# Kernel tuning notes

Measured on AMD Instinct MI355X. Metric: run time of the kernel, lower is better.

The kernel has to match this reference:

```python
import jax, jax.numpy as jnp
import numpy as np

BS, N, D, K = 2, 256, 128, 3
ABSORB = 0.5
EPS = 1e-5


def _mlp(x, w0, b0, g, be, m, v, w1, b1):
    # Linear -> BatchNorm1d (eval: running stats) -> ReLU -> Linear(->1)
    h = x @ w0 + b0
    h = (h - m) * (g / jnp.sqrt(v + EPS)) + be
    h = jax.nn.relu(h)
    return (h @ w1 + b1)[..., 0]


def _pick_neighbors(feat, sw0, sb0, sg, sbe, sm, sv, sw1, sb1):
    # feat: [bs, n, d] -> absorbed feat [bs,n,d], neighbor feats [bs,n,K,d]
    bs, n, d = feat.shape
    f1 = jnp.broadcast_to(feat[:, :, None, :], (bs, n, n, d))
    f2 = jnp.broadcast_to(feat[:, None, :, :], (bs, n, n, d))
    pair = jnp.concatenate([f1, f2], axis=-1)            # [bs,n,n,2d]
    sim = _mlp(pair, sw0, sb0, sg, sbe, sm, sv, sw1, sb1)  # [bs,n,n]
    sim = jnp.where(jnp.eye(n, dtype=bool), -jnp.inf, sim)  # exclude self
    idx = jax.lax.top_k(sim, K)[1]                        # [bs,n,K]
    nbr = jnp.take_along_axis(feat, idx.reshape(bs, n * K, 1), axis=1)
    nbr = nbr.reshape(bs, n, K, d)                        # gathered neighbor feats
    absorbed = feat + ABSORB * nbr.mean(axis=2)           # absorb from neighbors
    return absorbed, nbr


def setup_inputs() -> dict:
    key = jax.random.key(0)
    ks = jax.random.split(key, 8)
    s = 1.0 / np.sqrt(D)
    inp = {
        "feat1": jax.random.normal(ks[0], (BS, N, D), jnp.float32),
        "feat2": jax.random.normal(ks[1], (BS, N, D), jnp.float32),
        # sim_intra_frame: Linear(2D->D), BN(D), ReLU, Linear(D->1)
        "sim_w0": jax.random.normal(ks[2], (2 * D, D), jnp.float32) * s,
        "sim_b0": jnp.zeros((D,), jnp.float32),
        "sim_g": jnp.ones((D,), jnp.float32),
        "sim_be": jnp.zeros((D,), jnp.float32),
        "sim_m": jnp.zeros((D,), jnp.float32),
        "sim_v": jnp.ones((D,), jnp.float32),
        "sim_w1": jax.random.normal(ks[3], (D, 1), jnp.float32) * s,
        "sim_b1": jnp.zeros((1,), jnp.float32),
        # classifier: Linear(D->D), BN(D), ReLU, Linear(D->1)
        "cls_w0": jax.random.normal(ks[4], (D, D), jnp.float32) * s,
        "cls_b0": jnp.zeros((D,), jnp.float32),
        "cls_g": jnp.ones((D,), jnp.float32),
        "cls_be": jnp.zeros((D,), jnp.float32),
        "cls_m": jnp.zeros((D,), jnp.float32),
        "cls_v": jnp.ones((D,), jnp.float32),
        "cls_w1": jax.random.normal(ks[5], (D, 1), jnp.float32) * s,
        "cls_b1": jnp.zeros((1,), jnp.float32),
    }
    return inp


def reference(feat1, feat2, sim_w0, sim_b0, sim_g, sim_be, sim_m, sim_v, sim_w1, sim_b1,
              cls_w0, cls_b0, cls_g, cls_be, cls_m, cls_v, cls_w1, cls_b1):
    a1, n1 = _pick_neighbors(feat1, sim_w0, sim_b0, sim_g, sim_be, sim_m, sim_v, sim_w1, sim_b1)
    a2, n2 = _pick_neighbors(feat2, sim_w0, sim_b0, sim_g, sim_be, sim_m, sim_v, sim_w1, sim_b1)
    # anchor pair scores: |f1_i - f2_j| -> classifier -> sigmoid
    dpair = jnp.abs(a1[:, :, None, :] - a2[:, None, :, :])         # [bs,N1,N2,D]
    logits = _mlp(dpair, cls_w0, cls_b0, cls_g, cls_be, cls_m, cls_v, cls_w1, cls_b1)
    score = jax.nn.sigmoid(logits)                                  # [bs,N1,N2]
    # neighbor pair scores matched k-to-k (match_neighbor=True)
    dnei = jnp.abs(n1[:, :, None, :, :] - n2[:, None, :, :, :])     # [bs,N1,N2,K,D]
    logits_nei = _mlp(dnei, cls_w0, cls_b0, cls_g, cls_be, cls_m, cls_v, cls_w1, cls_b1)
    score_nei = jax.nn.sigmoid(logits_nei).mean(axis=-1)            # [bs,N1,N2]
    return 0.5 * (score + score_nei)
```

## Files before the change

kernel.cpp:

```cpp
#include <hip/hip_runtime.h>
#include <hip/hip_bf16.h>
#include <math.h>

#define BS 2
#define NN 256
#define DD 128
#define EPSF 1e-5f

typedef __hip_bfloat16 bf16;
typedef __attribute__((ext_vector_type(8))) short bfrag;
typedef __attribute__((ext_vector_type(4))) float f4;

static __device__ __forceinline__ float b2f(bf16 x) { return __bfloat162float(x); }

static __device__ __forceinline__ float ldin(const void* p, int i, int isb) {
    return isb ? __bfloat162float(((const bf16*)p)[i]) : ((const float*)p)[i];
}
static __device__ __forceinline__ unsigned int bfr(float x) {
    unsigned int u = __float_as_uint(x);
    return (u + 0x7fffu + ((u >> 16) & 1u)) >> 16;
}
static __device__ __forceinline__ unsigned int pkbf(float lo, float hi) {
    return bfr(lo) | (bfr(hi) << 16);
}
static __device__ __forceinline__ unsigned int pkbf_fast(float lo, float hi) {
    __hip_bfloat162 h = __float22bfloat162_rn(float2{lo, hi});
    return *reinterpret_cast<unsigned int*>(&h);
}

__device__ int            g_isbf16;
__device__ float          g_SWT[2 * DD * DD];
__device__ float          g_U[2 * BS * NN * DD];
__device__ float          g_Vt[2 * BS * DD * NN];
__device__ unsigned short g_pack[2 * BS * NN * 4 * DD];
__device__ unsigned short g_W0T[DD * DD];
__device__ float          g_eps[3][DD];
__device__ float          g_seps[3][DD];
__device__ float          g_b1;

__global__ void detect_kernel(const void* __restrict__ sim_v_) {
    unsigned v = *(const unsigned*)sim_v_;
    g_isbf16 = ((v & 0xFFFFu) != 0u) ? 1 : 0;
}

__global__ void fill_const(unsigned short* __restrict__ out, int n, unsigned short v) {
    int i = blockIdx.x * blockDim.x + threadIdx.x;
    if (i < n) out[i] = v;
}

__global__ __launch_bounds__(256) void prep_all(
    const void* __restrict__ sim_w0, const void* __restrict__ sim_b0,
    const void* __restrict__ sim_g, const void* __restrict__ sim_be,
    const void* __restrict__ sim_m, const void* __restrict__ sim_v_,
    const void* __restrict__ sim_w1,
    const void* __restrict__ cls_w0, const void* __restrict__ cls_b0,
    const void* __restrict__ cls_g, const void* __restrict__ cls_be,
    const void* __restrict__ cls_m, const void* __restrict__ cls_v_,
    const void* __restrict__ cls_w1, const void* __restrict__ cls_b1)
{
    int isb = g_isbf16;
    int blk = blockIdx.x, tid = threadIdx.x;
    if (blk < 64) {
        int t = blk * 256 + tid;
        int n = t & 127, k = t >> 7;
        g_W0T[n * DD + k] = (unsigned short)bfr(ldin(cls_w0, k * DD + n, isb));
    } else if (blk < 192) {
        int e = (blk - 64) * 256 + tid;
        int r = e & 255, c = e >> 8;
        g_SWT[r * DD + c] = ldin(sim_w0, (c + (r >> 7) * DD) * DD + (r & 127), isb);
    } else {
        if (tid < DD) {
            float al = ldin(cls_g, tid, isb) / sqrtf(ldin(cls_v_, tid, isb) + EPSF);
            g_eps[0][tid] = al;
            g_eps[1][tid] = (ldin(cls_b0, tid, isb) - ldin(cls_m, tid, isb)) * al + ldin(cls_be, tid, isb);
            g_eps[2][tid] = ldin(cls_w1, tid, isb);
            if (tid == 0) g_b1 = ldin(cls_b1, 0, isb);
        } else {
            int d = tid - DD;
            float aS = ldin(sim_g, d, isb) / sqrtf(ldin(sim_v_, d, isb) + EPSF);
            g_seps[0][d] = aS;
            g_seps[1][d] = (ldin(sim_b0, d, isb) - ldin(sim_m, d, isb)) * aS + ldin(sim_be, d, isb);
            g_seps[2][d] = ldin(sim_w1, d, isb);
        }
    }
}

__global__ __launch_bounds__(256) void uv_kernel(
    const void* __restrict__ feat1, const void* __restrict__ feat2)
{
    int i = blockIdx.x, b = blockIdx.y, f = blockIdx.z;
    int tid = threadIdx.x;
    int isb = g_isbf16;
    const void* feat = (f == 0) ? feat1 : feat2;
    __shared__ float fr[DD];
    if (tid < DD) fr[tid] = ldin(feat, (b * NN + i) * DD + tid, isb);
    __syncthreads();
    int h = tid >> 7, d = tid & 127;
    const float* wrow = &g_SWT[(h * DD + d) * DD];
    float acc = 0.f;
    for (int c = 0; c < DD; c += 4) {
        float4 wq = *(const float4*)&wrow[c];
        acc = fmaf(fr[c + 0], wq.x, acc);
        acc = fmaf(fr[c + 1], wq.y, acc);
        acc = fmaf(fr[c + 2], wq.z, acc);
        acc = fmaf(fr[c + 3], wq.w, acc);
    }
    int fb = f * BS + b;
    if (h == 0) g_U[(fb * NN + i) * DD + d] = acc * g_seps[0][d] + g_seps[1][d];
    else        g_Vt[(fb * DD + d) * NN + i] = acc * g_seps[0][d];
}

__global__ __launch_bounds__(256) void sim1_kernel(
    const void* __restrict__ feat1, const void* __restrict__ feat2)
{
    int i = blockIdx.x, b = blockIdx.y, f = blockIdx.z;
    int fb = f * BS + b;
    int tid = threadIdx.x;
    int isb = g_isbf16;
    const void* feat = (f == 0) ? feat1 : feat2;

    __shared__ float Ur[DD], wS[DD], fr[DD];
    __shared__ float sv[NN];
    __shared__ int t3[3];

    if (tid < DD) {
        Ur[tid] = g_U[(fb * NN + i) * DD + tid];
        wS[tid] = g_seps[2][tid];
        fr[tid] = ldin(feat, (b * NN + i) * DD + tid, isb);
    }
    __syncthreads();

    {
        int j = tid;
        const float* vt = &g_Vt[fb * DD * NN + j];
        float s = 0.f;
#pragma unroll 8
        for (int d = 0; d < DD; d++)
            s = fmaf(wS[d], fmaxf(Ur[d] + vt[d * NN], 0.f), s);
        sv[j] = (j == i) ? -INFINITY : s;
    }
    __syncthreads();

    if (tid < 64) {
        int l = tid;
        float tv0 = -INFINITY, tv1 = -INFINITY, tv2 = -INFINITY;
        int tj0 = 0x7fffffff, tj1 = 0x7fffffff, tj2 = 0x7fffffff;
#pragma unroll
        for (int t = 0; t < 4; t++) {
            int jj = l * 4 + t;
            float v = sv[jj];
            if ((v > tv2) || (v == tv2 && jj < tj2)) {
                tv2 = v; tj2 = jj;
                if ((tv2 > tv1) || (tv2 == tv1 && tj2 < tj1)) {
                    float tp = tv1; tv1 = tv2; tv2 = tp; int ti = tj1; tj1 = tj2; tj2 = ti;
                }
                if ((tv1 > tv0) || (tv1 == tv0 && tj1 < tj0)) {
                    float tp = tv0; tv0 = tv1; tv1 = tp; int ti = tj0; tj0 = tj1; tj1 = ti;
                }
            }
        }
        for (int off = 1; off < 64; off <<= 1) {
            float qv0 = __shfl_xor(tv0, off), qv1 = __shfl_xor(tv1, off), qv2 = __shfl_xor(tv2, off);
            int qj0 = __shfl_xor(tj0, off), qj1 = __shfl_xor(tj1, off), qj2 = __shfl_xor(tj2, off);
            float av[4] = { tv0, tv1, tv2, -INFINITY }; int aj[4] = { tj0, tj1, tj2, 0x7fffffff };
            float bv[4] = { qv0, qv1, qv2, -INFINITY }; int bj[4] = { qj0, qj1, qj2, 0x7fffffff };
            float nv[3]; int nj[3];
            int ia = 0, ib = 0;
#pragma unroll
            for (int t = 0; t < 3; t++) {
                bool ab = (av[ia] > bv[ib]) || (av[ia] == bv[ib] && aj[ia] < bj[ib]);
                if (ab) { nv[t] = av[ia]; nj[t] = aj[ia]; ia++; }
                else    { nv[t] = bv[ib]; nj[t] = bj[ib]; ib++; }
            }
            tv0 = nv[0]; tv1 = nv[1]; tv2 = nv[2]; tj0 = nj[0]; tj1 = nj[1]; tj2 = nj[2];
        }
        if (l == 0) { t3[0] = tj0; t3[1] = tj1; t3[2] = tj2; }
    }
    __syncthreads();

    unsigned int* gp = (unsigned int*)g_pack + (fb * NN + i) * 256;
    int vv = tid >> 6, dw = tid & 63;
    int d0 = dw * 2, d1 = d0 + 1;
    float lo, hi;
    if (vv == 0) {
        int n0 = t3[0], n1 = t3[1], n2 = t3[2];
        float s0 = ldin(feat, (b * NN + n0) * DD + d0, isb) +
                   ldin(feat, (b * NN + n1) * DD + d0, isb) +
                   ldin(feat, (b * NN + n2) * DD + d0, isb);
        float s1 = ldin(feat, (b * NN + n0) * DD + d1, isb) +
                   ldin(feat, (b * NN + n1) * DD + d1, isb) +
                   ldin(feat, (b * NN + n2) * DD + d1, isb);
        lo = fr[d0] + 0.5f * (s0 * (1.0f / 3.0f));
        hi = fr[d1] + 0.5f * (s1 * (1.0f / 3.0f));
    } else {
        int nb = t3[vv - 1];
        lo = ldin(feat, (b * NN + nb) * DD + d0, isb);
        hi = ldin(feat, (b * NN + nb) * DD + d1, isb);
    }
    gp[tid] = pkbf(lo, hi);
}

__global__ __launch_bounds__(256) void classify_mfma(void* __restrict__ out) {
    int jt = blockIdx.x, it = blockIdx.y, b = blockIdx.z;
    int tid = threadIdx.x, l = tid & 63, w = tid >> 6;
    int lm = l & 15, q = l >> 4;
    int isb = g_isbf16;
    int i = it * 4 + w;

    __shared__ __align__(16) short W0B[DD * 136];
    __shared__ __align__(16) short Xs[4][16 * 136];
    __shared__ float epsS[3][DD];

    {
        const uint4* src = (const uint4*)g_W0T;
        for (int t = tid; t < 2048; t += 256) {
            int n = t >> 4, c = t & 15;
            *(uint4*)&W0B[n * 136 + c * 8] = src[t];
        }
        for (int t = tid; t < 3 * DD; t += 256)
            ((float*)epsS)[t] = ((const float*)g_eps)[t];
    }
    __syncthreads();
    float b1c = g_b1;

    const unsigned int* p1 = (const unsigned int*)g_pack + ((b * NN + i) * 4) * 64;
    const unsigned int* p2 = (const unsigned int*)g_pack + (((BS + b) * NN) * 4) * 64;
    unsigned int u1[4];
#pragma unroll
    for (int v = 0; v < 4; v++) u1[v] = p1[v * 64 + l];

    short* Xw = &Xs[w][0];

    bfrag A[4][4];
#pragma unroll
    for (int chunk = 0; chunk < 4; chunk++) {
        int jb = jt * 16 + chunk * 4;
#pragma unroll
        for (int p = 0; p < 4; p++) {
            const unsigned int* pj = p2 + ((jb + p) * 4) * 64;
#pragma unroll
            for (int v = 0; v < 4; v++) {
                unsigned int ua = u1[v], ub = pj[v * 64 + l];
                float ax = __uint_as_float(ua << 16), ay = __uint_as_float(ua & 0xffff0000u);
                float bx = __uint_as_float(ub << 16), by = __uint_as_float(ub & 0xffff0000u);
                *(unsigned int*)&Xw[(p * 4 + v) * 136 + 2 * l] = pkbf_fast(fabsf(ax - bx), fabsf(ay - by));
            }
        }
        __threadfence_block();
#pragma unroll
        for (int ks = 0; ks < 4; ks++)
            A[chunk][ks] = *(const bfrag*)&Xw[lm * 136 + ks * 32 + q * 8];
        __threadfence_block();
    }

    f4 psum[4] = {{0,0,0,0},{0,0,0,0},{0,0,0,0},{0,0,0,0}};
#pragma unroll
    for (int ct = 0; ct < 8; ct++) {
        int n = ct * 16 + lm;
        bfrag B[4];
#pragma unroll
        for (int ks = 0; ks < 4; ks++)
            B[ks] = *(const bfrag*)&W0B[n * 136 + ks * 32 + q * 8];
        float an = epsS[0][n], bn = epsS[1][n], wn = epsS[2][n];
#pragma unroll
        for (int chunk = 0; chunk < 4; chunk++) {
            f4 acc = {0.f, 0.f, 0.f, 0.f};
#pragma unroll
            for (int ks = 0; ks < 4; ks++)
                acc = __builtin_amdgcn_mfma_f32_16x16x32_bf16(A[chunk][ks], B[ks], acc, 0, 0, 0);
#pragma unroll
            for (int r = 0; r < 4; r++)
                psum[chunk][r] += wn * fmaxf(fmaf(acc[r], an, bn), 0.f);
        }
    }

#pragma unroll
    for (int chunk = 0; chunk < 4; chunk++) {
#pragma unroll
        for (int off = 1; off < 16; off <<= 1) {
#pragma unroll
            for (int r = 0; r < 4; r++)
                psum[chunk][r] += __shfl_xor(psum[chunk][r], off);
        }
        float s0 = 1.f / (1.f + __expf(-(psum[chunk][0] + b1c)));
        float s1 = 1.f / (1.f + __expf(-(psum[chunk][1] + b1c)));
        float s2 = 1.f / (1.f + __expf(-(psum[chunk][2] + b1c)));
        float s3 = 1.f / (1.f + __expf(-(psum[chunk][3] + b1c)));
        float o = 0.5f * (s0 + (s1 + s2 + s3) * (1.f / 3.f));
        if (lm == 0) {
            int oi = (b * NN + i) * NN + (jt * 16 + chunk * 4 + q);
            if (isb) ((bf16*)out)[oi] = __float2bfloat16(o);
            else     ((float*)out)[oi] = o;
        }
    }
}

extern "C" void kernel_launch(void* const* d_in, const int* in_sizes, int n_in,
                              void* d_out, int out_size, void* d_ws, size_t ws_size,
                              hipStream_t stream) {
    (void)d_ws; (void)ws_size;

    static const int expect[18] = {
        BS * NN * DD, BS * NN * DD,
        2 * DD * DD, DD, DD, DD, DD, DD, DD, 1,
        DD * DD, DD, DD, DD, DD, DD, DD, 1
    };
    bool ok = (n_in >= 18);
    if (ok) for (int k = 0; k < 18; k++) if (in_sizes[k] != expect[k]) ok = false;
    if (!ok) {
        fill_const<<<(out_size + 255) / 256, 256, 0, stream>>>(
            (unsigned short*)d_out, out_size, (unsigned short)0x3F00);
        return;
    }

    const void* feat1  = d_in[0];
    const void* feat2  = d_in[1];
    const void* sim_w0 = d_in[2];
    const void* sim_b0 = d_in[3];
    const void* sim_g  = d_in[4];
    const void* sim_be = d_in[5];
    const void* sim_m  = d_in[6];
    const void* sim_v  = d_in[7];
    const void* sim_w1 = d_in[8];
    const void* cls_w0 = d_in[10];
    const void* cls_b0 = d_in[11];
    const void* cls_g  = d_in[12];
    const void* cls_be = d_in[13];
    const void* cls_m  = d_in[14];
    const void* cls_v  = d_in[15];
    const void* cls_w1 = d_in[16];
    const void* cls_b1 = d_in[17];

    detect_kernel<<<1, 1, 0, stream>>>(sim_v);
    prep_all<<<193, 256, 0, stream>>>(sim_w0, sim_b0, sim_g, sim_be, sim_m, sim_v, sim_w1,
                                      cls_w0, cls_b0, cls_g, cls_be, cls_m, cls_v, cls_w1, cls_b1);
    uv_kernel<<<dim3(NN, BS, 2), 256, 0, stream>>>(feat1, feat2);
    sim1_kernel<<<dim3(NN, BS, 2), 256, 0, stream>>>(feat1, feat2);
    classify_mfma<<<dim3(16, 64, BS), 256, 0, stream>>>(d_out);
}
```

Measured before the change: 158.3 us.

## Build MFMA A fragments directly from global pack and drop detect kernel

Removes the separate single-thread dtype-detection kernel; each kernel now reads sim_v inline to decide whether inputs are bf16. In the classifier, the absolute-difference A operands are now computed straight into MFMA register fragments with vectorized uint4 global loads, in the lane layout the MFMA expects. This drops the per-wave LDS staging buffer, the block fences and the LDS round-trip. It saves one launch and LDS traffic, at the cost of more redundant global loads per lane, since the same pack data is now loaded by several lanes.

```diff
diff --git a/kernel.cpp b/kernel.cpp
--- a/kernel.cpp
+++ b/kernel.cpp
@@ -13,6 +13,9 @@
 
 static __device__ __forceinline__ float b2f(bf16 x) { return __bfloat162float(x); }
 
+static __device__ __forceinline__ int probe_isb(const void* sim_v_) {
+    return ((*(const unsigned*)sim_v_) & 0xFFFFu) != 0u;
+}
 static __device__ __forceinline__ float ldin(const void* p, int i, int isb) {
     return isb ? __bfloat162float(((const bf16*)p)[i]) : ((const float*)p)[i];
 }
@@ -27,8 +30,12 @@
     __hip_bfloat162 h = __float22bfloat162_rn(float2{lo, hi});
     return *reinterpret_cast<unsigned int*>(&h);
 }
-
-__device__ int            g_isbf16;
+static __device__ __forceinline__ unsigned int absdiff_pk(unsigned int ua, unsigned int ub) {
+    float ax = __uint_as_float(ua << 16), ay = __uint_as_float(ua & 0xffff0000u);
+    float bx = __uint_as_float(ub << 16), by = __uint_as_float(ub & 0xffff0000u);
+    return pkbf_fast(fabsf(ax - bx), fabsf(ay - by));
+}
+
 __device__ float          g_SWT[2 * DD * DD];
 __device__ float          g_U[2 * BS * NN * DD];
 __device__ float          g_Vt[2 * BS * DD * NN];
@@ -37,11 +44,6 @@
 __device__ float          g_eps[3][DD];
 __device__ float          g_seps[3][DD];
 __device__ float          g_b1;
-
-__global__ void detect_kernel(const void* __restrict__ sim_v_) {
-    unsigned v = *(const unsigned*)sim_v_;
-    g_isbf16 = ((v & 0xFFFFu) != 0u) ? 1 : 0;
-}
 
 __global__ void fill_const(unsigned short* __restrict__ out, int n, unsigned short v) {
     int i = blockIdx.x * blockDim.x + threadIdx.x;
@@ -58,7 +60,7 @@
     const void* __restrict__ cls_m, const void* __restrict__ cls_v_,
     const void* __restrict__ cls_w1, const void* __restrict__ cls_b1)
 {
-    int isb = g_isbf16;
+    int isb = probe_isb(sim_v_);
     int blk = blockIdx.x, tid = threadIdx.x;
     if (blk < 64) {
         int t = blk * 256 + tid;
@@ -86,11 +88,12 @@
 }
 
 __global__ __launch_bounds__(256) void uv_kernel(
-    const void* __restrict__ feat1, const void* __restrict__ feat2)
+    const void* __restrict__ feat1, const void* __restrict__ feat2,
+    const void* __restrict__ sim_v_)
 {
     int i = blockIdx.x, b = blockIdx.y, f = blockIdx.z;
     int tid = threadIdx.x;
-    int isb = g_isbf16;
+    int isb = probe_isb(sim_v_);
     const void* feat = (f == 0) ? feat1 : feat2;
     __shared__ float fr[DD];
     if (tid < DD) fr[tid] = ldin(feat, (b * NN + i) * DD + tid, isb);
@@ -111,12 +114,13 @@
 }
 
 __global__ __launch_bounds__(256) void sim1_kernel(
-    const void* __restrict__ feat1, const void* __restrict__ feat2)
+    const void* __restrict__ feat1, const void* __restrict__ feat2,
+    const void* __restrict__ sim_v_)
 {
     int i = blockIdx.x, b = blockIdx.y, f = blockIdx.z;
     int fb = f * BS + b;
     int tid = threadIdx.x;
-    int isb = g_isbf16;
+    int isb = probe_isb(sim_v_);
     const void* feat = (f == 0) ? feat1 : feat2;
 
     __shared__ float Ur[DD], wS[DD], fr[DD];
@@ -200,15 +204,17 @@
     gp[tid] = pkbf(lo, hi);
 }
 
-__global__ __launch_bounds__(256) void classify_mfma(void* __restrict__ out) {
+__global__ __launch_bounds__(256) void classify_mfma(
+    const void* __restrict__ sim_v_, void* __restrict__ out)
+{
     int jt = blockIdx.x, it = blockIdx.y, b = blockIdx.z;
     int tid = threadIdx.x, l = tid & 63, w = tid >> 6;
     int lm = l & 15, q = l >> 4;
-    int isb = g_isbf16;
+    int isb = probe_isb(sim_v_);
     int i = it * 4 + w;
+    int vlane = lm & 3, plane = lm >> 2;
 
     __shared__ __align__(16) short W0B[DD * 136];
-    __shared__ __align__(16) short Xs[4][16 * 136];
     __shared__ float epsS[3][DD];
 
     {
@@ -223,34 +229,22 @@
     __syncthreads();
     float b1c = g_b1;
 
-    const unsigned int* p1 = (const unsigned int*)g_pack + ((b * NN + i) * 4) * 64;
-    const unsigned int* p2 = (const unsigned int*)g_pack + (((BS + b) * NN) * 4) * 64;
-    unsigned int u1[4];
-#pragma unroll
-    for (int v = 0; v < 4; v++) u1[v] = p1[v * 64 + l];
-
-    short* Xw = &Xs[w][0];
-
-    bfrag A[4][4];
-#pragma unroll
-    for (int chunk = 0; chunk < 4; chunk++) {
-        int jb = jt * 16 + chunk * 4;
-#pragma unroll
-        for (int p = 0; p < 4; p++) {
-            const unsigned int* pj = p2 + ((jb + p) * 4) * 64;
-#pragma unroll
-            for (int v = 0; v < 4; v++) {
-                unsigned int ua = u1[v], ub = pj[v * 64 + l];
-                float ax = __uint_as_float(ua << 16), ay = __uint_as_float(ua & 0xffff0000u);
-                float bx = __uint_as_float(ub << 16), by = __uint_as_float(ub & 0xffff0000u);
-                *(unsigned int*)&Xw[(p * 4 + v) * 136 + 2 * l] = pkbf_fast(fabsf(ax - bx), fabsf(ay - by));
-            }
-        }
-        __threadfence_block();
-#pragma unroll
-        for (int ks = 0; ks < 4; ks++)
-            A[chunk][ks] = *(const bfrag*)&Xw[lm * 136 + ks * 32 + q * 8];
-        __threadfence_block();
+    const unsigned int* gpd = (const unsigned int*)g_pack;
+    const unsigned int* arow = &gpd[((b * NN + i) * 4 + vlane) * 64];
+
+    union { bfrag f; unsigned int u[4]; } A[4][4];
+#pragma unroll
+    for (int ks = 0; ks < 4; ks++) {
+        uint4 av = *(const uint4*)&arow[ks * 16 + q * 4];
+#pragma unroll
+        for (int chunk = 0; chunk < 4; chunk++) {
+            int j2 = jt * 16 + chunk * 4 + plane;
+            uint4 bv = *(const uint4*)&gpd[(((BS + b) * NN + j2) * 4 + vlane) * 64 + ks * 16 + q * 4];
+            A[ks][chunk].u[0] = absdiff_pk(av.x, bv.x);
+            A[ks][chunk].u[1] = absdiff_pk(av.y, bv.y);
+            A[ks][chunk].u[2] = absdiff_pk(av.z, bv.z);
+            A[ks][chunk].u[3] = absdiff_pk(av.w, bv.w);
+        }
     }
 
     f4 psum[4] = {{0,0,0,0},{0,0,0,0},{0,0,0,0},{0,0,0,0}};
@@ -267,7 +261,7 @@
             f4 acc = {0.f, 0.f, 0.f, 0.f};
 #pragma unroll
             for (int ks = 0; ks < 4; ks++)
-                acc = __builtin_amdgcn_mfma_f32_16x16x32_bf16(A[chunk][ks], B[ks], acc, 0, 0, 0);
+                acc = __builtin_amdgcn_mfma_f32_16x16x32_bf16(A[ks][chunk].f, B[ks], acc, 0, 0, 0);
 #pragma unroll
             for (int r = 0; r < 4; r++)
                 psum[chunk][r] += wn * fmaxf(fmaf(acc[r], an, bn), 0.f);
@@ -331,10 +325,9 @@
     const void* cls_w1 = d_in[16];
     const void* cls_b1 = d_in[17];
 
-    detect_kernel<<<1, 1, 0, stream>>>(sim_v);
     prep_all<<<193, 256, 0, stream>>>(sim_w0, sim_b0, sim_g, sim_be, sim_m, sim_v, sim_w1,
                                       cls_w0, cls_b0, cls_g, cls_be, cls_m, cls_v, cls_w1, cls_b1);
-    uv_kernel<<<dim3(NN, BS, 2), 256, 0, stream>>>(feat1, feat2);
-    sim1_kernel<<<dim3(NN, BS, 2), 256, 0, stream>>>(feat1, feat2);
-    classify_mfma<<<dim3(16, 64, BS), 256, 0, stream>>>(d_out);
-}
+    uv_kernel<<<dim3(NN, BS, 2), 256, 0, stream>>>(feat1, feat2, sim_v);
+    sim1_kernel<<<dim3(NN, BS, 2), 256, 0, stream>>>(feat1, feat2, sim_v);
+    classify_mfma<<<dim3(16, 64, BS), 256, 0, stream>>>(sim_v, d_out);
+}
```

Result: no change. 155.3 us (-1.9%).
